# Performance work log

Measured on AMD Instinct MI355X. Metric: run time of the kernel, lower is better.

The kernel has to match this reference:

```python
import jax, jax.numpy as jnp
import numpy as np

B, S, D, H = 4, 2048, 512, 8
DK = D // H


def setup_inputs() -> dict:
    key = jax.random.key(0)
    k1, k2, k3, k4 = jax.random.split(key, 4)
    return {
        "Zq": jax.random.normal(k1, (B, S, D), dtype=jnp.float32),
        "Zkv": jax.random.normal(k2, (B, S, D), dtype=jnp.float32),
        "mask": jnp.zeros((1, 1, S, S), dtype=jnp.float32),
        "Wqkv": jax.random.normal(k3, (D, 3 * D), dtype=jnp.float32),
        "Wout": jax.random.normal(k4, (D, D), dtype=jnp.float32),
    }


def reference(Zq, Zkv, mask, Wqkv, Wout):
    d_k = Wqkv.shape[0] // H
    Wq, Wk, Wv = jnp.split(Wqkv, 3, axis=-1)
    b, s, d = Zq.shape
    # project and split heads: [B,S,D] -> [B,H,S,dk]
    Q = (Zq @ Wq).reshape(b, s, H, d_k).transpose(0, 2, 1, 3)
    K = (Zkv @ Wk).reshape(b, s, H, d_k).transpose(0, 2, 1, 3)
    V = (Zkv @ Wv).reshape(b, s, H, d_k).transpose(0, 2, 1, 3)
    scale = d_k ** -0.5
    scores = jnp.einsum("bhqd,bhkd->bhqk", Q, K) * scale + mask
    attn = jax.nn.softmax(scores, axis=-1)  # [B,H,Sq,Skv]
    ctx = jnp.einsum("bhqk,bhkd->bhqd", attn, V)
    out = ctx.transpose(0, 2, 1, 3).reshape(b, s, d) @ Wout
    return out, attn.mean(axis=1)
```

## Files before the change

kernel.cpp:

```cpp
#include <hip/hip_runtime.h>
#include <cstdint>

#define B_ 4
#define S_ 2048
#define D_ 512
#define H_ 8
#define DK_ 64
#define SCALE 0.125f
#define KSTR 84
#define PSTR 68

using bfrag = __attribute__((ext_vector_type(8))) __bf16;
using b4    = __attribute__((ext_vector_type(4))) __bf16;
using f4    = __attribute__((ext_vector_type(4))) float;

#define MFMA16(a, b, c) __builtin_amdgcn_mfma_f32_16x16x32_bf16(a, b, c, 0, 0, 0)

__global__ __launch_bounds__(256) void wtr(const float* __restrict__ W, int ldw, int c0,
                                           __bf16* __restrict__ th, __bf16* __restrict__ tl,
                                           int do_lo) {
  int idx = blockIdx.x * 256 + threadIdx.x;
  int k = idx & 511, n = idx >> 9;
  float x = W[(size_t)k * ldw + c0 + n];
  __bf16 h = (__bf16)x;
  th[(size_t)n * 512 + k] = h;
  if (do_lo) tl[(size_t)n * 512 + k] = (__bf16)(x - (float)h);
}

template <bool AF32, bool BF32, bool LO, int MODE>
__global__ __launch_bounds__(256) void gemm_mfma(
    const void* __restrict__ Ap, const void* __restrict__ Bp, const void* __restrict__ Blop,
    float* __restrict__ Cf, __bf16* __restrict__ Oh, __bf16* __restrict__ Ol) {
  __shared__ __bf16 Ash[64 * 40];
  __shared__ __bf16 Asl[64 * 40];
  __shared__ __bf16 Bsh[64 * 40];
  __shared__ __bf16 Bsl[64 * 40];

  const int tid = threadIdx.x;
  const int m0 = blockIdx.y * 64, n0 = blockIdx.x * 64;
  const int row = tid >> 2, seg = tid & 3;
  const int lane = tid & 63, wv = tid >> 6;
  const int wm = (wv & 1) * 32, wn = (wv >> 1) * 32;
  const int qd = lane >> 4, ln = lane & 15;

  f4 acc[2][2];
#pragma unroll
  for (int i = 0; i < 2; i++)
#pragma unroll
    for (int j = 0; j < 2; j++)
#pragma unroll
      for (int r = 0; r < 4; r++) acc[i][j][r] = 0.f;

  for (int kt = 0; kt < 512; kt += 32) {
    const size_t abase = (size_t)(m0 + row) * 512 + kt + seg * 8;
    const size_t bbase = (size_t)(n0 + row) * 512 + kt + seg * 8;
    float4 a0, a1, b0, b1, bl0;
    if constexpr (AF32) {
      const float* A = (const float*)Ap;
      a0 = *(const float4*)&A[abase];
      a1 = *(const float4*)&A[abase + 4];
    } else {
      const __bf16* A = (const __bf16*)Ap;
      a0 = *(const float4*)&A[abase];
    }
    if constexpr (BF32) {
      const float* Bm = (const float*)Bp;
      b0 = *(const float4*)&Bm[bbase];
      b1 = *(const float4*)&Bm[bbase + 4];
    } else {
      const __bf16* Bm = (const __bf16*)Bp;
      b0 = *(const float4*)&Bm[bbase];
      if constexpr (LO) {
        const __bf16* Bl = (const __bf16*)Blop;
        bl0 = *(const float4*)&Bl[bbase];
      }
    }
    __syncthreads();
    if constexpr (AF32) {
      float x[8] = {a0.x, a0.y, a0.z, a0.w, a1.x, a1.y, a1.z, a1.w};
      bfrag h, l;
#pragma unroll
      for (int j = 0; j < 8; j++) {
        h[j] = (__bf16)x[j];
        l[j] = (__bf16)(x[j] - (float)h[j]);
      }
      *(bfrag*)&Ash[row * 40 + seg * 8] = h;
      if constexpr (LO) *(bfrag*)&Asl[row * 40 + seg * 8] = l;
    } else {
      *(float4*)&Ash[row * 40 + seg * 8] = a0;
    }
    if constexpr (BF32) {
      float x[8] = {b0.x, b0.y, b0.z, b0.w, b1.x, b1.y, b1.z, b1.w};
      bfrag h;
#pragma unroll
      for (int j = 0; j < 8; j++) h[j] = (__bf16)x[j];
      *(bfrag*)&Bsh[row * 40 + seg * 8] = h;
    } else {
      *(float4*)&Bsh[row * 40 + seg * 8] = b0;
      if constexpr (LO) *(float4*)&Bsl[row * 40 + seg * 8] = bl0;
    }
    __syncthreads();

    bfrag ah[2], al[2], bh[2], bl[2];
#pragma unroll
    for (int mi = 0; mi < 2; mi++) {
      ah[mi] = *(bfrag*)&Ash[(wm + mi * 16 + ln) * 40 + qd * 8];
      if constexpr (LO) al[mi] = *(bfrag*)&Asl[(wm + mi * 16 + ln) * 40 + qd * 8];
    }
#pragma unroll
    for (int ni = 0; ni < 2; ni++) {
      bh[ni] = *(bfrag*)&Bsh[(wn + ni * 16 + ln) * 40 + qd * 8];
      if constexpr (LO) bl[ni] = *(bfrag*)&Bsl[(wn + ni * 16 + ln) * 40 + qd * 8];
    }
#pragma unroll
    for (int mi = 0; mi < 2; mi++)
#pragma unroll
      for (int ni = 0; ni < 2; ni++) {
        acc[mi][ni] = MFMA16(ah[mi], bh[ni], acc[mi][ni]);
        if constexpr (LO) {
          acc[mi][ni] = MFMA16(ah[mi], bl[ni], acc[mi][ni]);
          acc[mi][ni] = MFMA16(al[mi], bh[ni], acc[mi][ni]);
        }
      }
  }

#pragma unroll
  for (int mi = 0; mi < 2; mi++)
#pragma unroll
    for (int ni = 0; ni < 2; ni++)
#pragma unroll
      for (int r = 0; r < 4; r++) {
        const int mrow = m0 + wm + mi * 16 + qd * 4 + r;
        const int ncol = n0 + wn + ni * 16 + ln;
        const float c = acc[mi][ni][r];
        if constexpr (MODE == 0) {
          Cf[(size_t)mrow * 512 + ncol] = c;
        } else if constexpr (MODE == 1) {
          const int b = mrow >> 11, s = mrow & (S_ - 1);
          const int h = ncol >> 6, dk = ncol & 63;
          const size_t o = (((size_t)b * H_ + h) * S_ + s) * DK_ + dk;
          __bf16 hh = (__bf16)c;
          Oh[o] = hh;
          Ol[o] = (__bf16)(c - (float)hh);
        } else {
          const int h = mrow >> 6, dk = mrow & 63;
          const int b = ncol >> 11, s = ncol & (S_ - 1);
          Oh[(((size_t)b * H_ + h) * DK_ + dk) * S_ + s] = (__bf16)c;
        }
      }
}

__global__ __launch_bounds__(256) void attn_fctx(
    const __bf16* __restrict__ Qh_, const __bf16* __restrict__ Ql_,
    const __bf16* __restrict__ Kh_, const __bf16* __restrict__ Kl_,
    const __bf16* __restrict__ VT, const float* __restrict__ mask,
    __bf16* __restrict__ CTXb, float* __restrict__ MR, float* __restrict__ LR,
    __bf16* __restrict__ E, float* __restrict__ MT) {
  __shared__ __bf16 Ksh[64 * KSTR];
  __shared__ __bf16 Ksl[64 * KSTR];
  __shared__ __bf16 Vs[64 * KSTR];
  __shared__ __bf16 Ps[64 * PSTR];
  const int tid = threadIdx.x, lane = tid & 63, wv = tid >> 6;
  const int qd = lane >> 4, ln = lane & 15;
  const int bh = blockIdx.y;
  const int q0b = blockIdx.x * 64;
  const int q0w = q0b + wv * 16;
  const int srow = tid >> 2, sseg = tid & 3;

  bfrag qh[2], ql[2];
#pragma unroll
  for (int s = 0; s < 2; s++) {
    const size_t qb = ((size_t)bh * S_ + q0w + ln) * DK_ + s * 32 + qd * 8;
    qh[s] = *(const bfrag*)&Qh_[qb];
    ql[s] = *(const bfrag*)&Ql_[qb];
  }

  float m = -3.0e38f, l = 0.f;
  f4 cacc[4];
#pragma unroll
  for (int t = 0; t < 4; t++)
#pragma unroll
    for (int r = 0; r < 4; r++) cacc[t][r] = 0.f;

  float4 h0, h1, l0, l1, v0, v1;
  {
    const size_t kb = ((size_t)bh * S_ + srow) * DK_ + sseg * 16;
    const size_t vb = ((size_t)bh * DK_ + srow) * S_ + sseg * 16;
    h0 = *(const float4*)&Kh_[kb]; h1 = *(const float4*)&Kh_[kb + 8];
    l0 = *(const float4*)&Kl_[kb]; l1 = *(const float4*)&Kl_[kb + 8];
    v0 = *(const float4*)&VT[vb];  v1 = *(const float4*)&VT[vb + 8];
  }

  for (int kt = 0; kt < S_; kt += 64) {
    __syncthreads();
    *(float4*)&Ksh[srow * KSTR + sseg * 16] = h0;
    *(float4*)&Ksh[srow * KSTR + sseg * 16 + 8] = h1;
    *(float4*)&Ksl[srow * KSTR + sseg * 16] = l0;
    *(float4*)&Ksl[srow * KSTR + sseg * 16 + 8] = l1;
    *(float4*)&Vs[srow * KSTR + sseg * 16] = v0;
    *(float4*)&Vs[srow * KSTR + sseg * 16 + 8] = v1;
    __syncthreads();

    f4 mk[4];
#pragma unroll
    for (int t = 0; t < 4; t++)
      mk[t] = *(const f4*)&mask[(size_t)(q0w + ln) * S_ + kt + t * 16 + qd * 4];

    if (kt + 64 < S_) {
      const size_t kb = ((size_t)bh * S_ + kt + 64 + srow) * DK_ + sseg * 16;
      const size_t vb = ((size_t)bh * DK_ + srow) * S_ + kt + 64 + sseg * 16;
      h0 = *(const float4*)&Kh_[kb]; h1 = *(const float4*)&Kh_[kb + 8];
      l0 = *(const float4*)&Kl_[kb]; l1 = *(const float4*)&Kl_[kb + 8];
      v0 = *(const float4*)&VT[vb];  v1 = *(const float4*)&VT[vb + 8];
    }

    f4 z[4];
#pragma unroll
    for (int t = 0; t < 4; t++)
#pragma unroll
      for (int r = 0; r < 4; r++) z[t][r] = 0.f;
#pragma unroll
    for (int t = 0; t < 4; t++)
#pragma unroll
      for (int s = 0; s < 2; s++) {
        bfrag kbh = *(bfrag*)&Ksh[(t * 16 + ln) * KSTR + s * 32 + qd * 8];
        bfrag kbl = *(bfrag*)&Ksl[(t * 16 + ln) * KSTR + s * 32 + qd * 8];
        z[t] = MFMA16(kbh, qh[s], z[t]);
        z[t] = MFMA16(kbl, qh[s], z[t]);
        z[t] = MFMA16(kbh, ql[s], z[t]);
      }

    float zf[4][4];
#pragma unroll
    for (int t = 0; t < 4; t++)
#pragma unroll
      for (int r = 0; r < 4; r++)
        zf[t][r] = fmaf(z[t][r], SCALE, mk[t][r]);

    float tm = zf[0][0];
#pragma unroll
    for (int t = 0; t < 4; t++)
#pragma unroll
      for (int r = 0; r < 4; r++) tm = fmaxf(tm, zf[t][r]);
    tm = fmaxf(tm, __shfl_xor(tm, 16, 64));
    tm = fmaxf(tm, __shfl_xor(tm, 32, 64));
    const float nm = fmaxf(m, tm);
    const float al = __expf(m - nm);
    m = nm;

    float ls = 0.f;
#pragma unroll
    for (int t = 0; t < 4; t++) {
      float e0 = __expf(zf[t][0] - nm), e1 = __expf(zf[t][1] - nm);
      float e2 = __expf(zf[t][2] - nm), e3 = __expf(zf[t][3] - nm);
      ls += (e0 + e1) + (e2 + e3);
      b4 pk;
      pk[0] = (__bf16)e0; pk[1] = (__bf16)e1;
      pk[2] = (__bf16)e2; pk[3] = (__bf16)e3;
      *(b4*)&Ps[(wv * 16 + ln) * PSTR + t * 16 + qd * 4] = pk;
    }
    l = l * al + ls;

    if (qd == 0)
      MT[((size_t)bh * 32 + (kt >> 6)) * S_ + q0w + ln] = m;

    const float a0 = __shfl(al, qd * 4 + 0, 64);
    const float a1 = __shfl(al, qd * 4 + 1, 64);
    const float a2 = __shfl(al, qd * 4 + 2, 64);
    const float a3 = __shfl(al, qd * 4 + 3, 64);
#pragma unroll
    for (int t = 0; t < 4; t++) {
      cacc[t][0] *= a0; cacc[t][1] *= a1;
      cacc[t][2] *= a2; cacc[t][3] *= a3;
    }

    bfrag pa[2];
#pragma unroll
    for (int s = 0; s < 2; s++)
      pa[s] = *(bfrag*)&Ps[(wv * 16 + ln) * PSTR + s * 32 + qd * 8];
#pragma unroll
    for (int t = 0; t < 4; t++)
#pragma unroll
      for (int s = 0; s < 2; s++) {
        bfrag vbf = *(bfrag*)&Vs[(t * 16 + ln) * KSTR + s * 32 + qd * 8];
        cacc[t] = MFMA16(pa[s], vbf, cacc[t]);
      }

#pragma unroll
    for (int c = 0; c < 2; c++) {
      const int row = wv * 16 + (lane >> 3) + c * 8;
      const int ch = lane & 7;
      f4 ev = *(f4*)&Ps[row * PSTR + ch * 8];
      __builtin_nontemporal_store(
          ev, (f4*)&E[((size_t)bh * S_ + q0b + row) * S_ + kt + ch * 8]);
    }
  }

  l += __shfl_xor(l, 16, 64);
  l += __shfl_xor(l, 32, 64);
  const float inv = 1.0f / l;
  const float i0 = __shfl(inv, qd * 4 + 0, 64);
  const float i1 = __shfl(inv, qd * 4 + 1, 64);
  const float i2 = __shfl(inv, qd * 4 + 2, 64);
  const float i3 = __shfl(inv, qd * 4 + 3, 64);
  const int b = bh >> 3, h = bh & 7;
#pragma unroll
  for (int t = 0; t < 4; t++) {
    CTXb[((size_t)b * S_ + q0w + qd * 4 + 0) * D_ + h * DK_ + t * 16 + ln] = (__bf16)(cacc[t][0] * i0);
    CTXb[((size_t)b * S_ + q0w + qd * 4 + 1) * D_ + h * DK_ + t * 16 + ln] = (__bf16)(cacc[t][1] * i1);
    CTXb[((size_t)b * S_ + q0w + qd * 4 + 2) * D_ + h * DK_ + t * 16 + ln] = (__bf16)(cacc[t][2] * i2);
    CTXb[((size_t)b * S_ + q0w + qd * 4 + 3) * D_ + h * DK_ + t * 16 + ln] = (__bf16)(cacc[t][3] * i3);
  }
  if (qd == 0) {
    MR[(size_t)bh * S_ + q0w + ln] = m;
    LR[(size_t)bh * S_ + q0w + ln] = l;
  }
}

__global__ __launch_bounds__(256) void mean_rescale(
    const __bf16* __restrict__ E, const float* __restrict__ MT,
    const float* __restrict__ MR, const float* __restrict__ LR,
    float* __restrict__ meanout) {
  const int t = threadIdx.x;
  const int qr = t >> 3, seg = t & 7;
  const int b = blockIdx.y, ks = blockIdx.z;
  const int qg = blockIdx.x * 32 + qr;

  float mf[H_], il[H_];
#pragma unroll
  for (int h = 0; h < H_; h++) {
    const int bh = b * H_ + h;
    mf[h] = MR[(size_t)bh * S_ + qg];
    il[h] = 1.0f / LR[(size_t)bh * S_ + qg];
  }

  for (int kc = 0; kc < 8; kc++) {
    const int k0 = ks * 512 + kc * 64;
    const int tk = k0 >> 6;
    float acc[8];
#pragma unroll
    for (int j = 0; j < 8; j++) acc[j] = 0.f;
#pragma unroll
    for (int h = 0; h < H_; h++) {
      const int bh = b * H_ + h;
      const float mt = MT[((size_t)bh * 32 + tk) * S_ + qg];
      const float sc = __expf(mt - mf[h]) * il[h];
      bfrag e = __builtin_nontemporal_load(
          (const bfrag*)&E[((size_t)bh * S_ + qg) * S_ + k0 + seg * 8]);
#pragma unroll
      for (int j = 0; j < 8; j++) acc[j] += (float)e[j] * sc;
    }
    f4 o0, o1;
    o0[0] = acc[0] * 0.125f; o0[1] = acc[1] * 0.125f;
    o0[2] = acc[2] * 0.125f; o0[3] = acc[3] * 0.125f;
    o1[0] = acc[4] * 0.125f; o1[1] = acc[5] * 0.125f;
    o1[2] = acc[6] * 0.125f; o1[3] = acc[7] * 0.125f;
    float* mp = &meanout[((size_t)b * S_ + qg) * S_ + k0 + seg * 8];
    *(f4*)&mp[0] = o0;
    *(f4*)&mp[4] = o1;
  }
}

extern "C" void kernel_launch(void* const* d_in, const int* in_sizes, int n_in,
                              void* d_out, int out_size, void* d_ws, size_t ws_size,
                              hipStream_t stream) {
  (void)in_sizes; (void)n_in; (void)out_size; (void)ws_size;
  const float* Zq = (const float*)d_in[0];
  const float* Zkv = (const float*)d_in[1];
  const float* mask = (const float*)d_in[2];
  const float* Wqkv = (const float*)d_in[3];
  const float* Wout = (const float*)d_in[4];

  float* out = (float*)d_out;
  float* mean = out + (size_t)B_ * S_ * D_;

  char* w = (char*)d_ws;
  const size_t WSZ = 512 * 512 * sizeof(__bf16);
  const size_t QSZ = (size_t)B_ * H_ * S_ * DK_ * sizeof(__bf16);
  __bf16* WqTh = (__bf16*)w; w += WSZ;
  __bf16* WqTl = (__bf16*)w; w += WSZ;
  __bf16* WkTh = (__bf16*)w; w += WSZ;
  __bf16* WkTl = (__bf16*)w; w += WSZ;
  __bf16* WvTh = (__bf16*)w; w += WSZ;
  __bf16* WoTh = (__bf16*)w; w += WSZ;
  __bf16* Qh = (__bf16*)w; w += QSZ;
  __bf16* Ql = (__bf16*)w; w += QSZ;
  __bf16* Kh = (__bf16*)w; w += QSZ;
  __bf16* Kl = (__bf16*)w; w += QSZ;
  __bf16* VTh = (__bf16*)w; w += QSZ;
  __bf16* CTXb = (__bf16*)w; w += QSZ;
  float* MR = (float*)w; w += (size_t)B_ * H_ * S_ * sizeof(float);
  float* LR = (float*)w; w += (size_t)B_ * H_ * S_ * sizeof(float);
  float* MT = (float*)w; w += (size_t)B_ * H_ * 32 * S_ * sizeof(float);
  __bf16* E = (__bf16*)w; w += (size_t)B_ * H_ * S_ * S_ * sizeof(__bf16);

  wtr<<<1024, 256, 0, stream>>>(Wqkv, 1536, 0, WqTh, WqTl, 1);
  wtr<<<1024, 256, 0, stream>>>(Wqkv, 1536, 512, WkTh, WkTl, 1);
  wtr<<<1024, 256, 0, stream>>>(Wqkv, 1536, 1024, WvTh, nullptr, 0);
  wtr<<<1024, 256, 0, stream>>>(Wout, 512, 0, WoTh, nullptr, 0);

  gemm_mfma<true, false, true, 1><<<dim3(8, 128), 256, 0, stream>>>(
      Zq, WqTh, WqTl, nullptr, Qh, Ql);
  gemm_mfma<true, false, true, 1><<<dim3(8, 128), 256, 0, stream>>>(
      Zkv, WkTh, WkTl, nullptr, Kh, Kl);
  gemm_mfma<false, true, false, 2><<<dim3(128, 8), 256, 0, stream>>>(
      WvTh, Zkv, nullptr, nullptr, VTh, nullptr);

  attn_fctx<<<dim3(32, 32), 256, 0, stream>>>(Qh, Ql, Kh, Kl, VTh, mask, CTXb, MR, LR, E, MT);
  mean_rescale<<<dim3(64, 4, 4), 256, 0, stream>>>(E, MT, MR, LR, mean);

  gemm_mfma<false, false, false, 0><<<dim3(8, 128), 256, 0, stream>>>(
      CTXb, WoTh, nullptr, out, nullptr, nullptr);
}
```

Measured before the change: 413.8 us.

## Use 32x32 MFMA with 128-query attention tiles and fuse weight transposes

The attention kernel now gives each wave 32 query rows (128 per block) and computes QK^T with 32x32x16 MFMA, so each K/V tile loaded into shared memory serves twice as many queries. The per-row rescale factors move through a small shared array instead of lane shuffles, and PV runs as 2x4 16x16 tiles per wave. The four weight-transpose launches are merged into one launch. In exchange the grid has half as many blocks (512), which lowers parallelism, and register pressure and shared memory use go up.

```diff
diff --git a/kernel.cpp b/kernel.cpp
--- a/kernel.cpp
+++ b/kernel.cpp
@@ -13,18 +13,30 @@
 using bfrag = __attribute__((ext_vector_type(8))) __bf16;
 using b4    = __attribute__((ext_vector_type(4))) __bf16;
 using f4    = __attribute__((ext_vector_type(4))) float;
+using f16v  = __attribute__((ext_vector_type(16))) float;
 
 #define MFMA16(a, b, c) __builtin_amdgcn_mfma_f32_16x16x32_bf16(a, b, c, 0, 0, 0)
-
-__global__ __launch_bounds__(256) void wtr(const float* __restrict__ W, int ldw, int c0,
-                                           __bf16* __restrict__ th, __bf16* __restrict__ tl,
-                                           int do_lo) {
-  int idx = blockIdx.x * 256 + threadIdx.x;
-  int k = idx & 511, n = idx >> 9;
-  float x = W[(size_t)k * ldw + c0 + n];
-  __bf16 h = (__bf16)x;
+#define MFMA32(a, b, c) __builtin_amdgcn_mfma_f32_32x32x16_bf16(a, b, c, 0, 0, 0)
+
+__global__ __launch_bounds__(256) void wtr_all(
+    const float* __restrict__ Wqkv, const float* __restrict__ Wout,
+    __bf16* __restrict__ WqTh, __bf16* __restrict__ WqTl,
+    __bf16* __restrict__ WkTh, __bf16* __restrict__ WkTl,
+    __bf16* __restrict__ WvTh, __bf16* __restrict__ WoTh) {
+  const int by = blockIdx.y;
+  const int idx = blockIdx.x * 256 + threadIdx.x;
+  const int k = idx & 511, n = idx >> 9;
+  const float* W = (by == 3) ? Wout : Wqkv;
+  const int ldw = (by == 3) ? 512 : 1536;
+  const int c0 = (by == 3) ? 0 : by * 512;
+  const float x = W[(size_t)k * ldw + c0 + n];
+  const __bf16 h = (__bf16)x;
+  __bf16* th = (by == 0) ? WqTh : (by == 1) ? WkTh : (by == 2) ? WvTh : WoTh;
   th[(size_t)n * 512 + k] = h;
-  if (do_lo) tl[(size_t)n * 512 + k] = (__bf16)(x - (float)h);
+  if (by < 2) {
+    __bf16* tl = (by == 0) ? WqTl : WkTl;
+    tl[(size_t)n * 512 + k] = (__bf16)(x - (float)h);
+  }
 }
 
 template <bool AF32, bool BF32, bool LO, int MODE>
@@ -159,28 +171,32 @@
   __shared__ __bf16 Ksh[64 * KSTR];
   __shared__ __bf16 Ksl[64 * KSTR];
   __shared__ __bf16 Vs[64 * KSTR];
-  __shared__ __bf16 Ps[64 * PSTR];
+  __shared__ __bf16 Ps[128 * PSTR];
+  __shared__ float als[128];
   const int tid = threadIdx.x, lane = tid & 63, wv = tid >> 6;
+  const int l31 = lane & 31, kh = lane >> 5;
   const int qd = lane >> 4, ln = lane & 15;
   const int bh = blockIdx.y;
-  const int q0b = blockIdx.x * 64;
-  const int q0w = q0b + wv * 16;
+  const int q0b = blockIdx.x * 128;
+  const int q0w = q0b + wv * 32;
   const int srow = tid >> 2, sseg = tid & 3;
 
-  bfrag qh[2], ql[2];
-#pragma unroll
-  for (int s = 0; s < 2; s++) {
-    const size_t qb = ((size_t)bh * S_ + q0w + ln) * DK_ + s * 32 + qd * 8;
-    qh[s] = *(const bfrag*)&Qh_[qb];
-    ql[s] = *(const bfrag*)&Ql_[qb];
+  bfrag qhf[4], qlf[4];
+#pragma unroll
+  for (int ks = 0; ks < 4; ks++) {
+    const size_t qb = ((size_t)bh * S_ + q0w + l31) * DK_ + ks * 16 + kh * 8;
+    qhf[ks] = *(const bfrag*)&Qh_[qb];
+    qlf[ks] = *(const bfrag*)&Ql_[qb];
   }
 
   float m = -3.0e38f, l = 0.f;
-  f4 cacc[4];
-#pragma unroll
-  for (int t = 0; t < 4; t++)
-#pragma unroll
-    for (int r = 0; r < 4; r++) cacc[t][r] = 0.f;
+  f4 cacc[2][4];
+#pragma unroll
+  for (int mt = 0; mt < 2; mt++)
+#pragma unroll
+    for (int nt = 0; nt < 4; nt++)
+#pragma unroll
+      for (int r = 0; r < 4; r++) cacc[mt][nt][r] = 0.f;
 
   float4 h0, h1, l0, l1, v0, v1;
   {
@@ -201,10 +217,12 @@
     *(float4*)&Vs[srow * KSTR + sseg * 16 + 8] = v1;
     __syncthreads();
 
-    f4 mk[4];
-#pragma unroll
-    for (int t = 0; t < 4; t++)
-      mk[t] = *(const f4*)&mask[(size_t)(q0w + ln) * S_ + kt + t * 16 + qd * 4];
+    f4 mk[2][4];
+#pragma unroll
+    for (int t = 0; t < 2; t++)
+#pragma unroll
+      for (int g = 0; g < 4; g++)
+        mk[t][g] = *(const f4*)&mask[(size_t)(q0w + l31) * S_ + kt + t * 32 + g * 8 + 4 * kh];
 
     if (kt + 64 < S_) {
       const size_t kb = ((size_t)bh * S_ + kt + 64 + srow) * DK_ + sseg * 16;
@@ -214,81 +232,87 @@
       v0 = *(const float4*)&VT[vb];  v1 = *(const float4*)&VT[vb + 8];
     }
 
-    f4 z[4];
-#pragma unroll
-    for (int t = 0; t < 4; t++)
-#pragma unroll
-      for (int r = 0; r < 4; r++) z[t][r] = 0.f;
-#pragma unroll
-    for (int t = 0; t < 4; t++)
-#pragma unroll
-      for (int s = 0; s < 2; s++) {
-        bfrag kbh = *(bfrag*)&Ksh[(t * 16 + ln) * KSTR + s * 32 + qd * 8];
-        bfrag kbl = *(bfrag*)&Ksl[(t * 16 + ln) * KSTR + s * 32 + qd * 8];
-        z[t] = MFMA16(kbh, qh[s], z[t]);
-        z[t] = MFMA16(kbl, qh[s], z[t]);
-        z[t] = MFMA16(kbh, ql[s], z[t]);
-      }
-
-    float zf[4][4];
-#pragma unroll
-    for (int t = 0; t < 4; t++)
-#pragma unroll
-      for (int r = 0; r < 4; r++)
-        zf[t][r] = fmaf(z[t][r], SCALE, mk[t][r]);
-
-    float tm = zf[0][0];
-#pragma unroll
-    for (int t = 0; t < 4; t++)
-#pragma unroll
-      for (int r = 0; r < 4; r++) tm = fmaxf(tm, zf[t][r]);
-    tm = fmaxf(tm, __shfl_xor(tm, 16, 64));
+    f16v z[2];
+#pragma unroll
+    for (int t = 0; t < 2; t++)
+#pragma unroll
+      for (int r = 0; r < 16; r++) z[t][r] = 0.f;
+#pragma unroll
+    for (int t = 0; t < 2; t++)
+#pragma unroll
+      for (int ks = 0; ks < 4; ks++) {
+        bfrag kbh = *(bfrag*)&Ksh[(t * 32 + l31) * KSTR + ks * 16 + kh * 8];
+        bfrag kbl = *(bfrag*)&Ksl[(t * 32 + l31) * KSTR + ks * 16 + kh * 8];
+        z[t] = MFMA32(kbh, qhf[ks], z[t]);
+        z[t] = MFMA32(kbl, qhf[ks], z[t]);
+        z[t] = MFMA32(kbh, qlf[ks], z[t]);
+      }
+
+#pragma unroll
+    for (int t = 0; t < 2; t++)
+#pragma unroll
+      for (int r = 0; r < 16; r++)
+        z[t][r] = fmaf(z[t][r], SCALE, mk[t][r >> 2][r & 3]);
+
+    float tm = z[0][0];
+#pragma unroll
+    for (int t = 0; t < 2; t++)
+#pragma unroll
+      for (int r = 0; r < 16; r++) tm = fmaxf(tm, z[t][r]);
     tm = fmaxf(tm, __shfl_xor(tm, 32, 64));
     const float nm = fmaxf(m, tm);
     const float al = __expf(m - nm);
     m = nm;
+    if (lane < 32) als[wv * 32 + lane] = al;
 
     float ls = 0.f;
 #pragma unroll
-    for (int t = 0; t < 4; t++) {
-      float e0 = __expf(zf[t][0] - nm), e1 = __expf(zf[t][1] - nm);
-      float e2 = __expf(zf[t][2] - nm), e3 = __expf(zf[t][3] - nm);
-      ls += (e0 + e1) + (e2 + e3);
-      b4 pk;
-      pk[0] = (__bf16)e0; pk[1] = (__bf16)e1;
-      pk[2] = (__bf16)e2; pk[3] = (__bf16)e3;
-      *(b4*)&Ps[(wv * 16 + ln) * PSTR + t * 16 + qd * 4] = pk;
-    }
+    for (int t = 0; t < 2; t++)
+#pragma unroll
+      for (int g = 0; g < 4; g++) {
+        const float e0 = __expf(z[t][g * 4 + 0] - nm);
+        const float e1 = __expf(z[t][g * 4 + 1] - nm);
+        const float e2 = __expf(z[t][g * 4 + 2] - nm);
+        const float e3 = __expf(z[t][g * 4 + 3] - nm);
+        ls += (e0 + e1) + (e2 + e3);
+        b4 pk;
+        pk[0] = (__bf16)e0; pk[1] = (__bf16)e1;
+        pk[2] = (__bf16)e2; pk[3] = (__bf16)e3;
+        *(b4*)&Ps[(wv * 32 + l31) * PSTR + t * 32 + g * 8 + 4 * kh] = pk;
+      }
     l = l * al + ls;
 
-    if (qd == 0)
-      MT[((size_t)bh * 32 + (kt >> 6)) * S_ + q0w + ln] = m;
-
-    const float a0 = __shfl(al, qd * 4 + 0, 64);
-    const float a1 = __shfl(al, qd * 4 + 1, 64);
-    const float a2 = __shfl(al, qd * 4 + 2, 64);
-    const float a3 = __shfl(al, qd * 4 + 3, 64);
-#pragma unroll
-    for (int t = 0; t < 4; t++) {
-      cacc[t][0] *= a0; cacc[t][1] *= a1;
-      cacc[t][2] *= a2; cacc[t][3] *= a3;
-    }
-
-    bfrag pa[2];
-#pragma unroll
-    for (int s = 0; s < 2; s++)
-      pa[s] = *(bfrag*)&Ps[(wv * 16 + ln) * PSTR + s * 32 + qd * 8];
-#pragma unroll
-    for (int t = 0; t < 4; t++)
-#pragma unroll
-      for (int s = 0; s < 2; s++) {
-        bfrag vbf = *(bfrag*)&Vs[(t * 16 + ln) * KSTR + s * 32 + qd * 8];
-        cacc[t] = MFMA16(pa[s], vbf, cacc[t]);
-      }
-
-#pragma unroll
-    for (int c = 0; c < 2; c++) {
-      const int row = wv * 16 + (lane >> 3) + c * 8;
+    if (lane < 32)
+      MT[((size_t)bh * 32 + (kt >> 6)) * S_ + q0w + lane] = m;
+
+#pragma unroll
+    for (int mt = 0; mt < 2; mt++) {
+      f4 av = *(f4*)&als[wv * 32 + mt * 16 + qd * 4];
+#pragma unroll
+      for (int nt = 0; nt < 4; nt++)
+#pragma unroll
+        for (int r = 0; r < 4; r++) cacc[mt][nt][r] *= av[r];
+    }
+
+    bfrag pa[2][2];
+#pragma unroll
+    for (int mt = 0; mt < 2; mt++)
+#pragma unroll
+      for (int ks = 0; ks < 2; ks++)
+        pa[mt][ks] = *(bfrag*)&Ps[(wv * 32 + mt * 16 + ln) * PSTR + ks * 32 + qd * 8];
+#pragma unroll
+    for (int nt = 0; nt < 4; nt++)
+#pragma unroll
+      for (int ks = 0; ks < 2; ks++) {
+        bfrag vbf = *(bfrag*)&Vs[(nt * 16 + ln) * KSTR + ks * 32 + qd * 8];
+#pragma unroll
+        for (int mt = 0; mt < 2; mt++)
+          cacc[mt][nt] = MFMA16(pa[mt][ks], vbf, cacc[mt][nt]);
+      }
+
+#pragma unroll
+    for (int c = 0; c < 4; c++) {
+      const int row = wv * 32 + (lane >> 3) + c * 8;
       const int ch = lane & 7;
       f4 ev = *(f4*)&Ps[row * PSTR + ch * 8];
       __builtin_nontemporal_store(
@@ -296,24 +320,22 @@
     }
   }
 
-  l += __shfl_xor(l, 16, 64);
   l += __shfl_xor(l, 32, 64);
-  const float inv = 1.0f / l;
-  const float i0 = __shfl(inv, qd * 4 + 0, 64);
-  const float i1 = __shfl(inv, qd * 4 + 1, 64);
-  const float i2 = __shfl(inv, qd * 4 + 2, 64);
-  const float i3 = __shfl(inv, qd * 4 + 3, 64);
+  if (lane < 32) {
+    MR[(size_t)bh * S_ + q0w + lane] = m;
+    LR[(size_t)bh * S_ + q0w + lane] = l;
+    als[wv * 32 + lane] = 1.0f / l;
+  }
   const int b = bh >> 3, h = bh & 7;
 #pragma unroll
-  for (int t = 0; t < 4; t++) {
-    CTXb[((size_t)b * S_ + q0w + qd * 4 + 0) * D_ + h * DK_ + t * 16 + ln] = (__bf16)(cacc[t][0] * i0);
-    CTXb[((size_t)b * S_ + q0w + qd * 4 + 1) * D_ + h * DK_ + t * 16 + ln] = (__bf16)(cacc[t][1] * i1);
-    CTXb[((size_t)b * S_ + q0w + qd * 4 + 2) * D_ + h * DK_ + t * 16 + ln] = (__bf16)(cacc[t][2] * i2);
-    CTXb[((size_t)b * S_ + q0w + qd * 4 + 3) * D_ + h * DK_ + t * 16 + ln] = (__bf16)(cacc[t][3] * i3);
-  }
-  if (qd == 0) {
-    MR[(size_t)bh * S_ + q0w + ln] = m;
-    LR[(size_t)bh * S_ + q0w + ln] = l;
+  for (int mt = 0; mt < 2; mt++) {
+    f4 iv = *(f4*)&als[wv * 32 + mt * 16 + qd * 4];
+#pragma unroll
+    for (int nt = 0; nt < 4; nt++)
+#pragma unroll
+      for (int r = 0; r < 4; r++)
+        CTXb[((size_t)b * S_ + q0w + mt * 16 + qd * 4 + r) * D_ + h * DK_ + nt * 16 + ln] =
+            (__bf16)(cacc[mt][nt][r] * iv[r]);
   }
 }
 
@@ -394,10 +416,7 @@
   float* MT = (float*)w; w += (size_t)B_ * H_ * 32 * S_ * sizeof(float);
   __bf16* E = (__bf16*)w; w += (size_t)B_ * H_ * S_ * S_ * sizeof(__bf16);
 
-  wtr<<<1024, 256, 0, stream>>>(Wqkv, 1536, 0, WqTh, WqTl, 1);
-  wtr<<<1024, 256, 0, stream>>>(Wqkv, 1536, 512, WkTh, WkTl, 1);
-  wtr<<<1024, 256, 0, stream>>>(Wqkv, 1536, 1024, WvTh, nullptr, 0);
-  wtr<<<1024, 256, 0, stream>>>(Wout, 512, 0, WoTh, nullptr, 0);
+  wtr_all<<<dim3(1024, 4), 256, 0, stream>>>(Wqkv, Wout, WqTh, WqTl, WkTh, WkTl, WvTh, WoTh);
 
   gemm_mfma<true, false, true, 1><<<dim3(8, 128), 256, 0, stream>>>(
       Zq, WqTh, WqTl, nullptr, Qh, Ql);
@@ -406,7 +425,7 @@
   gemm_mfma<false, true, false, 2><<<dim3(128, 8), 256, 0, stream>>>(
       WvTh, Zkv, nullptr, nullptr, VTh, nullptr);
 
-  attn_fctx<<<dim3(32, 32), 256, 0, stream>>>(Qh, Ql, Kh, Kl, VTh, mask, CTXb, MR, LR, E, MT);
+  attn_fctx<<<dim3(16, 32), 256, 0, stream>>>(Qh, Ql, Kh, Kl, VTh, mask, CTXb, MR, LR, E, MT);
   mean_rescale<<<dim3(64, 4, 4), 256, 0, stream>>>(E, MT, MR, LR, mean);
 
   gemm_mfma<false, false, false, 0><<<dim3(8, 128), 256, 0, stream>>>(
```

Result: faster. 390.2 us (-5.7%).
